# Performance work log

Hardware: AMD Instinct MI355X
Metric: run time of the kernel (lower is better)

The kernel has to match this reference:

```python
import jax, jax.numpy as jnp
import numpy as np

D = 512      # d_model
S = 8        # num_quantum_states
B, T = 16, 1024
LN_EPS = 1e-5


def setup_inputs() -> dict:
    key = jax.random.key(0)
    ks = jax.random.split(key, 10)
    sc = lambda fan_in: 1.0 / np.sqrt(fan_in)
    return {
        "x": jax.random.normal(ks[0], (B, T, D), dtype=jnp.float32),
        # entanglement gates: torch Linear weight [out=D, in=2D], bias [D], stacked over S
        "W_ent": jax.random.uniform(ks[1], (S, D, 2 * D), minval=-sc(2 * D), maxval=sc(2 * D)),
        "b_ent": jax.random.uniform(ks[2], (S, D), minval=-sc(2 * D), maxval=sc(2 * D)),
        # measurement MLP: Linear(D*S->D), LayerNorm(D), Tanh, Linear(D->1)
        "m1_w": jax.random.uniform(ks[3], (D, D * S), minval=-sc(D * S), maxval=sc(D * S)),
        "m1_b": jax.random.uniform(ks[4], (D,), minval=-sc(D * S), maxval=sc(D * S)),
        "ln_g": jnp.ones((D,), dtype=jnp.float32),
        "ln_b": jnp.zeros((D,), dtype=jnp.float32),
        "m2_w": jax.random.uniform(ks[5], (1, D), minval=-sc(D), maxval=sc(D)),
        "m2_b": jax.random.uniform(ks[6], (1,), minval=-sc(D), maxval=sc(D)),
    }


def _layernorm(h, g, b):
    mu = jnp.mean(h, axis=-1, keepdims=True)
    var = jnp.mean(jnp.square(h - mu), axis=-1, keepdims=True)
    return (h - mu) * jax.lax.rsqrt(var + LN_EPS) * g + b


def reference(x, W_ent, b_ent, m1_w, m1_b, ln_g, ln_b, m2_w, m2_b):
    b_, t_, d_ = x.shape
    s_ = W_ent.shape[0]
    # gate(cat[x_i, x_j]).mean(dim=2) == x_i @ W1^T + mean_j(x_j) @ W2^T + b  (exact algebra)
    W1 = W_ent[:, :, :d_]   # [S, D, D] acts on x_i
    W2 = W_ent[:, :, d_:]   # [S, D, D] acts on x_j (mean over j)
    xbar = jnp.mean(x, axis=1)                                   # [B, D]
    ent = (jnp.einsum('btd,sed->bste', x, W1)                    # [B, S, T, D]
           + jnp.einsum('bd,sed->bse', xbar, W2)[:, :, None, :]
           + b_ent[None, :, None, :])
    # permute(0,2,3,1).reshape(B,T,D*S): feature layout is (d, s) fastest on s
    qv = jnp.transpose(ent, (0, 2, 3, 1)).reshape(b_, t_, d_ * s_)
    h = jnp.tanh(_layernorm(qv @ m1_w.T + m1_b, ln_g, ln_b))     # [B, T, D]
    attn_logits = h @ m2_w.T + m2_b                              # [B, T, 1]
    attn_weights = jax.nn.softmax(attn_logits, axis=1)
    context = jnp.sum(attn_weights * x, axis=1)                  # [B, D]
    return context, attn_weights
```

## Files before the change

### kernel.cpp

```cpp
#include <hip/hip_runtime.h>
#include <hip/hip_bf16.h>

typedef __attribute__((ext_vector_type(8))) short bf16x8;
typedef __attribute__((ext_vector_type(4))) float f32x4;

__device__ __forceinline__ float bf2f(unsigned short u) {
    union { unsigned int i; float f; } c; c.i = ((unsigned int)u) << 16; return c.f;
}
__device__ __forceinline__ unsigned short f2bf(float f) {
    union { float f; unsigned int i; } c; c.f = f;
    unsigned int x = c.i;
    x += 0x7fffu + ((x >> 16) & 1u);
    return (unsigned short)(x >> 16);
}
__device__ __forceinline__ float tanh_fast(float v) {
    float a = fabsf(v);
    a = fminf(a, 15.0f);
    float e = __expf(2.0f * a);
    float t = 1.0f - 2.0f / (e + 1.0f);
    return copysignf(t, v);
}

#define GLOAD_LDS16(gp, lp) \
    __builtin_amdgcn_global_load_lds((const __attribute__((address_space(1))) void*)(gp), \
                                     (__attribute__((address_space(3))) void*)(lp), 16, 0, 0)

#define MFMA(a, b, c) __builtin_amdgcn_mfma_f32_16x16x32_bf16((a), (b), (c), 0, 0, 0)


__global__ void k_sumx(const float* __restrict__ x, float* __restrict__ sumx) {
    int b = blockIdx.x, tc = blockIdx.y;
    int tid = threadIdx.x;
    const float* xp = x + ((size_t)b * 1024 + tc * 64) * 512;
    float a0 = 0.f, a1 = 0.f;
    for (int t = 0; t < 64; ++t) {
        a0 += xp[(size_t)t * 512 + tid];
        a1 += xp[(size_t)t * 512 + tid + 256];
    }
    atomicAdd(&sumx[b * 512 + tid], a0);
    atomicAdd(&sumx[b * 512 + tid + 256], a1);
}

__global__ void k_prepA(const float* __restrict__ m1w, const float* __restrict__ bent,
                        unsigned short* __restrict__ Abf, float* __restrict__ bias2) {
    int i = blockIdx.x, tid = threadIdx.x;
    const float* row = m1w + (size_t)i * 4096;
    float acc = 0.f;
    #pragma unroll
    for (int q = 0; q < 4; ++q) {
        int col = q * 1024 + tid * 4;
        float4 v = *(const float4*)(row + col);
        ushort4 o;
        o.x = f2bf(v.x); o.y = f2bf(v.y); o.z = f2bf(v.z); o.w = f2bf(v.w);
        *(ushort4*)(Abf + (size_t)i * 4096 + col) = o;
        int e0 = col >> 3, s0 = col & 7;
        acc += v.x * bent[(s0    ) * 512 + e0];
        acc += v.y * bent[(s0 + 1) * 512 + e0];
        acc += v.z * bent[(s0 + 2) * 512 + e0];
        acc += v.w * bent[(s0 + 3) * 512 + e0];
    }
    #pragma unroll
    for (int off = 32; off; off >>= 1) acc += __shfl_xor(acc, off);
    __shared__ float r4[4];
    if ((tid & 63) == 0) r4[tid >> 6] = acc;
    __syncthreads();
    if (tid == 0) bias2[i] = r4[0] + r4[1] + r4[2] + r4[3];
}

__global__ void k_conv_W(const float* __restrict__ W, unsigned short* __restrict__ WT) {
    __shared__ float tile[128][33];
    int e0 = blockIdx.x * 16;
    int j0 = blockIdx.y * 32;
    int tid = threadIdx.x;
    int tx = tid & 31, ty = tid >> 5;
    #pragma unroll
    for (int q = 0; q < 16; ++q) {
        int lk = q * 8 + ty;
        int de = lk >> 3, s = lk & 7;
        int r = s * 512 + e0 + de;
        tile[lk][tx] = W[(size_t)r * 1024 + j0 + tx];
    }
    __syncthreads();
    int j = tid >> 3, ck = (tid & 7) * 16;
    unsigned short* dst = WT + (size_t)(j0 + j) * 4096 + e0 * 8 + ck;
    #pragma unroll
    for (int g = 0; g < 4; ++g) {
        ushort4 o;
        o.x = f2bf(tile[ck + g * 4 + 0][j]);
        o.y = f2bf(tile[ck + g * 4 + 1][j]);
        o.z = f2bf(tile[ck + g * 4 + 2][j]);
        o.w = f2bf(tile[ck + g * 4 + 3][j]);
        *(ushort4*)(dst + g * 4) = o;
    }
}

__launch_bounds__(512, 2)
__global__ void k_gemm1(const unsigned short* __restrict__ Abf,
                        const unsigned short* __restrict__ WT,
                        float* __restrict__ CpL, float* __restrict__ CpR) {
    __shared__ __align__(16) unsigned short sA[64 * 64];
    __shared__ __align__(16) unsigned short sB[256 * 64];
    int i0 = blockIdx.x * 64;
    int j0 = blockIdx.y * 256;
    int kbase = blockIdx.z * 512;
    int tid = threadIdx.x, lane = tid & 63, w = tid >> 6;
    int wm = w >> 2, wn = w & 3;
    int lr = lane >> 3, sl = lane & 7;
    int lo = lane & 15, hi = lane >> 4;
    int arow = w * 8 + lr;
    const unsigned short* gA = Abf + (size_t)(i0 + arow) * 4096 + kbase + ((sl ^ lr) << 3);
    unsigned short* dA = sA + w * 8 * 64;
    const unsigned short* gB[4]; unsigned short* dB[4];
    #pragma unroll
    for (int g = 0; g < 4; ++g) {
        int brow = w * 32 + g * 8 + lr;
        gB[g] = WT + (size_t)(j0 + brow) * 4096 + kbase + ((sl ^ lr) << 3);
        dB[g] = sB + (w * 32 + g * 8) * 64;
    }
    bool left = (blockIdx.y < 2);
    f32x4 acc[2][4] = {};
    for (int k0 = 0; k0 < 512; k0 += 64) {
        if (k0) __syncthreads();
        GLOAD_LDS16(gA + k0, dA);
        #pragma unroll
        for (int g = 0; g < 4; ++g) GLOAD_LDS16(gB[g] + k0, dB[g]);
        __syncthreads();
        #pragma unroll
        for (int kk = 0; kk < 2; ++kk) {
            int slotX = ((kk * 4 + hi) ^ (lo & 7)) << 3;
            bf16x8 a0 = *(const bf16x8*)(sA + (wm * 32 +      lo) * 64 + slotX);
            bf16x8 a1 = *(const bf16x8*)(sA + (wm * 32 + 16 + lo) * 64 + slotX);
            #pragma unroll
            for (int n = 0; n < 4; ++n) {
                bf16x8 bb = *(const bf16x8*)(sB + (wn * 64 + n * 16 + lo) * 64 + slotX);
                if (left) {
                    acc[0][n] = MFMA(a0, bb, acc[0][n]);
                    acc[1][n] = MFMA(a1, bb, acc[1][n]);
                } else {
                    acc[0][n] = MFMA(bb, a0, acc[0][n]);
                    acc[1][n] = MFMA(bb, a1, acc[1][n]);
                }
            }
        }
    }
    int ksoff = blockIdx.z * 262144;
    if (left) {
        #pragma unroll
        for (int m = 0; m < 2; ++m) {
            int ib = i0 + wm * 32 + m * 16 + hi * 4;
            #pragma unroll
            for (int n = 0; n < 4; ++n) {
                int j = j0 + wn * 64 + n * 16 + lo;
                #pragma unroll
                for (int r = 0; r < 4; ++r)
                    CpL[ksoff + (ib + r) * 512 + j] = acc[m][n][r];
            }
        }
    } else {
        #pragma unroll
        for (int m = 0; m < 2; ++m) {
            int ic = i0 + wm * 32 + m * 16 + lo;
            #pragma unroll
            for (int n = 0; n < 4; ++n) {
                int db = j0 - 512 + wn * 64 + n * 16 + hi * 4;
                #pragma unroll
                for (int r = 0; r < 4; ++r)
                    CpR[ksoff + (db + r) * 512 + ic] = acc[m][n][r];
            }
        }
    }
}

__global__ void k_reduce8(const float* __restrict__ Cp, unsigned short* __restrict__ outbf) {
    int gid = blockIdx.x * 256 + threadIdx.x;
    float4 s = ((const float4*)Cp)[gid];
    #pragma unroll
    for (int ks = 1; ks < 8; ++ks) {
        float4 t = ((const float4*)Cp)[ks * 65536 + gid];
        s.x += t.x; s.y += t.y; s.z += t.z; s.w += t.w;
    }
    ushort4 o;
    o.x = f2bf(s.x); o.y = f2bf(s.y); o.z = f2bf(s.z); o.w = f2bf(s.w);
    ((ushort4*)outbf)[gid] = o;
}

__global__ void k_cb(const float* __restrict__ sumx, const unsigned short* __restrict__ M2t,
                     const float* __restrict__ bias2, const float* __restrict__ m1b,
                     float* __restrict__ cbo) {
    int b = blockIdx.x, i0 = blockIdx.y * 64;
    int tid = threadIdx.x;
    int il = tid & 63, dq = tid >> 6;
    const float* sx = sumx + b * 512 + dq * 128;
    const unsigned short* mp = M2t + (size_t)dq * 128 * 512 + i0 + il;
    float acc = 0.f;
    #pragma unroll 4
    for (int dd = 0; dd < 128; ++dd)
        acc += sx[dd] * bf2f(mp[(size_t)dd * 512]);
    __shared__ float sPart[4][64];
    sPart[dq][il] = acc;
    __syncthreads();
    if (tid < 64) {
        float v = sPart[0][tid] + sPart[1][tid] + sPart[2][tid] + sPart[3][tid];
        cbo[b * 512 + i0 + tid] = v * (1.0f / 1024.0f) + bias2[i0 + tid] + m1b[i0 + tid];
    }
}

__launch_bounds__(512, 2)
__global__ void k_gemm2(const float* __restrict__ x,
                        const unsigned short* __restrict__ M1bf,
                        const float* __restrict__ cb,
                        const float* __restrict__ lng, const float* __restrict__ lnb,
                        const float* __restrict__ m2w, const float* __restrict__ m2b,
                        float* __restrict__ logits) {
    __shared__ __align__(16) unsigned short sA[64 * 64];
    __shared__ __align__(16) unsigned short sB[512 * 64];
    __shared__ float sRed[2][8][64];
    __shared__ float sMu[64], sRs[64];
    __shared__ float sLp[8][64];
    int bt0 = blockIdx.x * 64;
    int b = bt0 >> 10;
    int tid = threadIdx.x, lane = tid & 63, w = tid >> 6;
    int wm = w >> 2, wn = w & 3;
    int lo = lane & 15, hi = lane >> 4;
    int lr = lane >> 3, sl = lane & 7;
    int arow = tid >> 3, aslot = tid & 7;
    const float* gA = x + (size_t)(bt0 + arow) * 512 + aslot * 8;
    unsigned short* dAp = sA + arow * 64 + ((aslot ^ (arow & 7)) << 3);
    const unsigned short* gB[8]; unsigned short* dB[8];
    #pragma unroll
    for (int g = 0; g < 8; ++g) {
        int brow = w * 64 + g * 8 + lr;
        gB[g] = M1bf + (size_t)brow * 512 + ((sl ^ lr) << 3);
        dB[g] = sB + (w * 64 + g * 8) * 64;
    }
    f32x4 acc[2][8] = {};
    for (int k0 = 0; k0 < 512; k0 += 64) {
        if (k0) __syncthreads();
        #pragma unroll
        for (int g = 0; g < 8; ++g) GLOAD_LDS16(gB[g] + k0, dB[g]);
        float4 f0 = *(const float4*)(gA + k0);
        float4 f1 = *(const float4*)(gA + k0 + 4);
        bf16x8 pk;
        pk[0] = (short)f2bf(f0.x); pk[1] = (short)f2bf(f0.y);
        pk[2] = (short)f2bf(f0.z); pk[3] = (short)f2bf(f0.w);
        pk[4] = (short)f2bf(f1.x); pk[5] = (short)f2bf(f1.y);
        pk[6] = (short)f2bf(f1.z); pk[7] = (short)f2bf(f1.w);
        *(bf16x8*)dAp = pk;
        __syncthreads();
        #pragma unroll
        for (int kk = 0; kk < 2; ++kk) {
            int slotX = ((kk * 4 + hi) ^ (lo & 7)) << 3;
            bf16x8 a0 = *(const bf16x8*)(sA + (wm * 32 +      lo) * 64 + slotX);
            bf16x8 a1 = *(const bf16x8*)(sA + (wm * 32 + 16 + lo) * 64 + slotX);
            #pragma unroll
            for (int n = 0; n < 8; ++n) {
                bf16x8 bb = *(const bf16x8*)(sB + (wn * 128 + n * 16 + lo) * 64 + slotX);
                acc[0][n] = MFMA(a0, bb, acc[0][n]);
                acc[1][n] = MFMA(a1, bb, acc[1][n]);
            }
        }
    }
    #pragma unroll
    for (int n = 0; n < 8; ++n) {
        float cbv = cb[b * 512 + wn * 128 + n * 16 + lo];
        #pragma unroll
        for (int m = 0; m < 2; ++m)
            #pragma unroll
            for (int r = 0; r < 4; ++r)
                acc[m][n][r] += cbv;
    }
    #pragma unroll
    for (int m = 0; m < 2; ++m) {
        #pragma unroll
        for (int r = 0; r < 4; ++r) {
            float s1 = 0.f, s2 = 0.f;
            #pragma unroll
            for (int n = 0; n < 8; ++n) { float t = acc[m][n][r]; s1 += t; s2 += t * t; }
            #pragma unroll
            for (int msk = 1; msk < 16; msk <<= 1) {
                s1 += __shfl_xor(s1, msk);
                s2 += __shfl_xor(s2, msk);
            }
            if (lo == 0) {
                int row = wm * 32 + m * 16 + hi * 4 + r;
                sRed[0][w][row] = s1;
                sRed[1][w][row] = s2;
            }
        }
    }
    __syncthreads();
    if (tid < 64) {
        int wmr = tid >> 5;
        float s1 = 0.f, s2 = 0.f;
        #pragma unroll
        for (int q = 0; q < 4; ++q) { s1 += sRed[0][wmr * 4 + q][tid]; s2 += sRed[1][wmr * 4 + q][tid]; }
        float mu = s1 * (1.0f / 512.0f);
        float var = s2 * (1.0f / 512.0f) - mu * mu;
        sMu[tid] = mu;
        sRs[tid] = rsqrtf(var + 1e-5f);
    }
    __syncthreads();
    float gv[8], bv[8], wv[8];
    #pragma unroll
    for (int n = 0; n < 8; ++n) {
        int c = wn * 128 + n * 16 + lo;
        gv[n] = lng[c]; bv[n] = lnb[c]; wv[n] = m2w[c];
    }
    #pragma unroll
    for (int m = 0; m < 2; ++m) {
        #pragma unroll
        for (int r = 0; r < 4; ++r) {
            int row = wm * 32 + m * 16 + hi * 4 + r;
            float mu = sMu[row], rs = sRs[row];
            float lg = 0.f;
            #pragma unroll
            for (int n = 0; n < 8; ++n) {
                float h = tanh_fast((acc[m][n][r] - mu) * rs * gv[n] + bv[n]);
                lg += h * wv[n];
            }
            #pragma unroll
            for (int msk = 1; msk < 16; msk <<= 1) lg += __shfl_xor(lg, msk);
            if (lo == 0) sLp[w][row] = lg;
        }
    }
    __syncthreads();
    if (tid < 64) {
        int wmr = tid >> 5;
        float lg = 0.f;
        #pragma unroll
        for (int q = 0; q < 4; ++q) lg += sLp[wmr * 4 + q][tid];
        logits[bt0 + tid] = lg + m2b[0];
    }
}

__global__ void k_softmax(const float* __restrict__ logits, float* __restrict__ wout) {
    int b = blockIdx.x, tid = threadIdx.x;
    __shared__ float red[4];
    float4 v = ((const float4*)(logits + b * 1024))[tid];
    float mx = fmaxf(fmaxf(v.x, v.y), fmaxf(v.z, v.w));
    for (int off = 32; off; off >>= 1) mx = fmaxf(mx, __shfl_xor(mx, off));
    if ((tid & 63) == 0) red[tid >> 6] = mx;
    __syncthreads();
    mx = fmaxf(fmaxf(red[0], red[1]), fmaxf(red[2], red[3]));
    float e0 = expf(v.x - mx), e1 = expf(v.y - mx), e2 = expf(v.z - mx), e3 = expf(v.w - mx);
    float sm = e0 + e1 + e2 + e3;
    for (int off = 32; off; off >>= 1) sm += __shfl_xor(sm, off);
    __syncthreads();
    if ((tid & 63) == 0) red[tid >> 6] = sm;
    __syncthreads();
    float inv = 1.0f / (red[0] + red[1] + red[2] + red[3]);
    float4 o; o.x = e0 * inv; o.y = e1 * inv; o.z = e2 * inv; o.w = e3 * inv;
    ((float4*)(wout + b * 1024))[tid] = o;
}

__global__ void k_context(const float* __restrict__ x, const float* __restrict__ wts,
                          float* __restrict__ ctx) {
    int b = blockIdx.x, tc = blockIdx.y;
    int tid = threadIdx.x;
    const float* xp = x + ((size_t)b * 1024 + tc * 64) * 512;
    const float* wp = wts + b * 1024 + tc * 64;
    float a0 = 0.f, a1 = 0.f;
    for (int t = 0; t < 64; ++t) {
        float wv = wp[t];
        a0 += wv * xp[(size_t)t * 512 + tid];
        a1 += wv * xp[(size_t)t * 512 + tid + 256];
    }
    atomicAdd(&ctx[b * 512 + tid], a0);
    atomicAdd(&ctx[b * 512 + tid + 256], a1);
}

extern "C" void kernel_launch(void* const* d_in, const int* in_sizes, int n_in,
                              void* d_out, int out_size, void* d_ws, size_t ws_size,
                              hipStream_t stream) {
    (void)in_sizes; (void)n_in; (void)out_size; (void)ws_size;
    const float* x    = (const float*)d_in[0];
    const float* Went = (const float*)d_in[1];
    const float* bent = (const float*)d_in[2];
    const float* m1w  = (const float*)d_in[3];
    const float* m1b  = (const float*)d_in[4];
    const float* lng  = (const float*)d_in[5];
    const float* lnb  = (const float*)d_in[6];
    const float* m2w  = (const float*)d_in[7];
    const float* m2b  = (const float*)d_in[8];
    float* out = (float*)d_out;
    char* ws = (char*)d_ws;

    unsigned short* Abf   = (unsigned short*)(ws);
    unsigned short* WT    = (unsigned short*)(ws + 4194304);
    float* CpL            = (float*)(ws + 12582912);
    float* CpR            = (float*)(ws + 20971520);
    unsigned short* M1bf  = (unsigned short*)(ws + 29360128);
    unsigned short* M2t   = (unsigned short*)(ws + 29884416);
    float* sumx   = (float*)(ws + 30408704);
    float* bias2  = (float*)(ws + 30441472);
    float* cb     = (float*)(ws + 30443520);
    float* logits = (float*)(ws + 30476288);

    hipMemsetAsync(sumx, 0, 512 * 16 * sizeof(float), stream);
    hipMemsetAsync(out, 0, 8192 * sizeof(float), stream);

    k_sumx<<<dim3(16, 16), 256, 0, stream>>>(x, sumx);
    k_prepA<<<512, 256, 0, stream>>>(m1w, bent, Abf, bias2);
    k_conv_W<<<dim3(32, 32), 256, 0, stream>>>(Went, WT);
    k_gemm1<<<dim3(8, 4, 8), 512, 0, stream>>>(Abf, WT, CpL, CpR);
    k_reduce8<<<256, 256, 0, stream>>>(CpL, M1bf);
    k_reduce8<<<256, 256, 0, stream>>>(CpR, M2t);
    k_cb<<<dim3(16, 8), 256, 0, stream>>>(sumx, M2t, bias2, m1b, cb);
    k_gemm2<<<256, 512, 0, stream>>>(x, M1bf, cb, lng, lnb, m2w, m2b, logits);
    k_softmax<<<16, 256, 0, stream>>>(logits, out + 8192);
    k_context<<<dim3(16, 16), 256, 0, stream>>>(x, out + 8192, out);
}
```

Before: 93.73 us.

## Double-buffer LDS in both GEMMs and merge the two reduce launches

Both MFMA GEMM kernels now keep two LDS buffers and issue the global-to-LDS loads for the next k-tile before computing on the current one. Explicit vmcnt waits, raw barriers, sched barriers and setprio around the MFMA block control the ordering. The two split-K reduce launches are merged into one grid of 512 blocks. In exchange, gemm2 doubles its LDS use (about 72 KB per block), which may cut occupancy, and its launch bound drops the min-blocks hint. The hand-counted vmcnt values must stay in step with the number of loads issued.

New measurement: 90.34 us. -3.6%, faster.

```diff
diff --git a/kernel.cpp b/kernel.cpp
--- a/kernel.cpp
+++ b/kernel.cpp
@@ -26,6 +26,9 @@
                                      (__attribute__((address_space(3))) void*)(lp), 16, 0, 0)
 
 #define MFMA(a, b, c) __builtin_amdgcn_mfma_f32_16x16x32_bf16((a), (b), (c), 0, 0, 0)
+
+#define SBAR()  __builtin_amdgcn_s_barrier()
+#define SCHED0() __builtin_amdgcn_sched_barrier(0)
 
 
 __global__ void k_sumx(const float* __restrict__ x, float* __restrict__ sumx) {
@@ -98,8 +101,8 @@
 __global__ void k_gemm1(const unsigned short* __restrict__ Abf,
                         const unsigned short* __restrict__ WT,
                         float* __restrict__ CpL, float* __restrict__ CpR) {
-    __shared__ __align__(16) unsigned short sA[64 * 64];
-    __shared__ __align__(16) unsigned short sB[256 * 64];
+    __shared__ __align__(16) unsigned short sA[2][64 * 64];
+    __shared__ __align__(16) unsigned short sB[2][256 * 64];
     int i0 = blockIdx.x * 64;
     int j0 = blockIdx.y * 256;
     int kbase = blockIdx.z * 512;
@@ -109,30 +112,44 @@
     int lo = lane & 15, hi = lane >> 4;
     int arow = w * 8 + lr;
     const unsigned short* gA = Abf + (size_t)(i0 + arow) * 4096 + kbase + ((sl ^ lr) << 3);
-    unsigned short* dA = sA + w * 8 * 64;
-    const unsigned short* gB[4]; unsigned short* dB[4];
-    #pragma unroll
-    for (int g = 0; g < 4; ++g) {
-        int brow = w * 32 + g * 8 + lr;
-        gB[g] = WT + (size_t)(j0 + brow) * 4096 + kbase + ((sl ^ lr) << 3);
-        dB[g] = sB + (w * 32 + g * 8) * 64;
-    }
+    const unsigned short* gB0 = WT + (size_t)(j0 + w * 32 + 0 * 8 + lr) * 4096 + kbase + ((sl ^ lr) << 3);
+    const unsigned short* gB1 = WT + (size_t)(j0 + w * 32 + 1 * 8 + lr) * 4096 + kbase + ((sl ^ lr) << 3);
+    const unsigned short* gB2 = WT + (size_t)(j0 + w * 32 + 2 * 8 + lr) * 4096 + kbase + ((sl ^ lr) << 3);
+    const unsigned short* gB3 = WT + (size_t)(j0 + w * 32 + 3 * 8 + lr) * 4096 + kbase + ((sl ^ lr) << 3);
     bool left = (blockIdx.y < 2);
     f32x4 acc[2][4] = {};
-    for (int k0 = 0; k0 < 512; k0 += 64) {
-        if (k0) __syncthreads();
-        GLOAD_LDS16(gA + k0, dA);
-        #pragma unroll
-        for (int g = 0; g < 4; ++g) GLOAD_LDS16(gB[g] + k0, dB[g]);
-        __syncthreads();
+
+#define G1_STAGE(tt, bufn)                                                    \
+    do {                                                                      \
+        int koff = (tt) * 64;                                                 \
+        GLOAD_LDS16(gA + koff, &sA[bufn][w * 8 * 64]);                        \
+        GLOAD_LDS16(gB0 + koff, &sB[bufn][(w * 32 + 0) * 64]);                \
+        GLOAD_LDS16(gB1 + koff, &sB[bufn][(w * 32 + 8) * 64]);                \
+        GLOAD_LDS16(gB2 + koff, &sB[bufn][(w * 32 + 16) * 64]);               \
+        GLOAD_LDS16(gB3 + koff, &sB[bufn][(w * 32 + 24) * 64]);               \
+        SCHED0();                                                             \
+    } while (0)
+
+    G1_STAGE(0, 0);
+    #pragma unroll
+    for (int t = 0; t < 8; ++t) {
+        int buf = t & 1;
+        if (t < 7) {
+            G1_STAGE(t + 1, buf ^ 1);
+            asm volatile("s_waitcnt vmcnt(5)" ::: "memory");
+        } else {
+            asm volatile("s_waitcnt vmcnt(0)" ::: "memory");
+        }
+        SCHED0(); SBAR(); SCHED0();
+        __builtin_amdgcn_s_setprio(1);
         #pragma unroll
         for (int kk = 0; kk < 2; ++kk) {
             int slotX = ((kk * 4 + hi) ^ (lo & 7)) << 3;
-            bf16x8 a0 = *(const bf16x8*)(sA + (wm * 32 +      lo) * 64 + slotX);
-            bf16x8 a1 = *(const bf16x8*)(sA + (wm * 32 + 16 + lo) * 64 + slotX);
+            bf16x8 a0 = *(const bf16x8*)(&sA[buf][(wm * 32 +      lo) * 64 + slotX]);
+            bf16x8 a1 = *(const bf16x8*)(&sA[buf][(wm * 32 + 16 + lo) * 64 + slotX]);
             #pragma unroll
             for (int n = 0; n < 4; ++n) {
-                bf16x8 bb = *(const bf16x8*)(sB + (wn * 64 + n * 16 + lo) * 64 + slotX);
+                bf16x8 bb = *(const bf16x8*)(&sB[buf][(wn * 64 + n * 16 + lo) * 64 + slotX]);
                 if (left) {
                     acc[0][n] = MFMA(a0, bb, acc[0][n]);
                     acc[1][n] = MFMA(a1, bb, acc[1][n]);
@@ -142,7 +159,11 @@
                 }
             }
         }
-    }
+        __builtin_amdgcn_s_setprio(0);
+        if (t < 7) { SCHED0(); SBAR(); SCHED0(); }
+    }
+#undef G1_STAGE
+
     int ksoff = blockIdx.z * 262144;
     if (left) {
         #pragma unroll
@@ -171,8 +192,12 @@
     }
 }
 
-__global__ void k_reduce8(const float* __restrict__ Cp, unsigned short* __restrict__ outbf) {
-    int gid = blockIdx.x * 256 + threadIdx.x;
+__global__ void k_reduce(const float* __restrict__ CpL, const float* __restrict__ CpR,
+                         unsigned short* __restrict__ M1bf, unsigned short* __restrict__ M2t) {
+    int bx = blockIdx.x;
+    const float* Cp = (bx < 256) ? CpL : CpR;
+    unsigned short* ob = (bx < 256) ? M1bf : M2t;
+    int gid = (bx & 255) * 256 + threadIdx.x;
     float4 s = ((const float4*)Cp)[gid];
     #pragma unroll
     for (int ks = 1; ks < 8; ++ks) {
@@ -181,7 +206,7 @@
     }
     ushort4 o;
     o.x = f2bf(s.x); o.y = f2bf(s.y); o.z = f2bf(s.z); o.w = f2bf(s.w);
-    ((ushort4*)outbf)[gid] = o;
+    ((ushort4*)ob)[gid] = o;
 }
 
 __global__ void k_cb(const float* __restrict__ sumx, const unsigned short* __restrict__ M2t,
@@ -205,15 +230,15 @@
     }
 }
 
-__launch_bounds__(512, 2)
+__launch_bounds__(512)
 __global__ void k_gemm2(const float* __restrict__ x,
                         const unsigned short* __restrict__ M1bf,
                         const float* __restrict__ cb,
                         const float* __restrict__ lng, const float* __restrict__ lnb,
                         const float* __restrict__ m2w, const float* __restrict__ m2b,
                         float* __restrict__ logits) {
-    __shared__ __align__(16) unsigned short sA[64 * 64];
-    __shared__ __align__(16) unsigned short sB[512 * 64];
+    __shared__ __align__(16) unsigned short sA[2][64 * 64];
+    __shared__ __align__(16) unsigned short sB[2][512 * 64];
     __shared__ float sRed[2][8][64];
     __shared__ float sMu[64], sRs[64];
     __shared__ float sLp[8][64];
@@ -225,41 +250,77 @@
     int lr = lane >> 3, sl = lane & 7;
     int arow = tid >> 3, aslot = tid & 7;
     const float* gA = x + (size_t)(bt0 + arow) * 512 + aslot * 8;
-    unsigned short* dAp = sA + arow * 64 + ((aslot ^ (arow & 7)) << 3);
-    const unsigned short* gB[8]; unsigned short* dB[8];
-    #pragma unroll
-    for (int g = 0; g < 8; ++g) {
-        int brow = w * 64 + g * 8 + lr;
-        gB[g] = M1bf + (size_t)brow * 512 + ((sl ^ lr) << 3);
-        dB[g] = sB + (w * 64 + g * 8) * 64;
-    }
+    int aoff = arow * 64 + ((aslot ^ (arow & 7)) << 3);
+    const unsigned short* gB[8];
+    #pragma unroll
+    for (int g = 0; g < 8; ++g)
+        gB[g] = M1bf + (size_t)(w * 64 + g * 8 + lr) * 512 + ((sl ^ lr) << 3);
+    float4 pf0, pf1;
     f32x4 acc[2][8] = {};
-    for (int k0 = 0; k0 < 512; k0 += 64) {
-        if (k0) __syncthreads();
-        #pragma unroll
-        for (int g = 0; g < 8; ++g) GLOAD_LDS16(gB[g] + k0, dB[g]);
-        float4 f0 = *(const float4*)(gA + k0);
-        float4 f1 = *(const float4*)(gA + k0 + 4);
-        bf16x8 pk;
-        pk[0] = (short)f2bf(f0.x); pk[1] = (short)f2bf(f0.y);
-        pk[2] = (short)f2bf(f0.z); pk[3] = (short)f2bf(f0.w);
-        pk[4] = (short)f2bf(f1.x); pk[5] = (short)f2bf(f1.y);
-        pk[6] = (short)f2bf(f1.z); pk[7] = (short)f2bf(f1.w);
-        *(bf16x8*)dAp = pk;
-        __syncthreads();
+
+#define G2_ISSUE(tt, bufn)                                                    \
+    do {                                                                      \
+        pf0 = *(const float4*)(gA + (tt) * 64);                               \
+        pf1 = *(const float4*)(gA + (tt) * 64 + 4);                           \
+        SCHED0();                                                             \
+        _Pragma("unroll")                                                     \
+        for (int g = 0; g < 8; ++g)                                           \
+            GLOAD_LDS16(gB[g] + (tt) * 64, &sB[bufn][(w * 64 + g * 8) * 64]); \
+        SCHED0();                                                             \
+    } while (0)
+
+#define G2_AWRITE(bufn)                                                      \
+    do {                                                                     \
+        bf16x8 pk;                                                           \
+        pk[0] = (short)f2bf(pf0.x); pk[1] = (short)f2bf(pf0.y);              \
+        pk[2] = (short)f2bf(pf0.z); pk[3] = (short)f2bf(pf0.w);              \
+        pk[4] = (short)f2bf(pf1.x); pk[5] = (short)f2bf(pf1.y);              \
+        pk[6] = (short)f2bf(pf1.z); pk[7] = (short)f2bf(pf1.w);              \
+        *(bf16x8*)(&sA[bufn][aoff]) = pk;                                    \
+    } while (0)
+
+    G2_ISSUE(0, 0);
+    asm volatile("s_waitcnt vmcnt(8)" ::: "memory");
+    SCHED0();
+    G2_AWRITE(0);
+    asm volatile("s_waitcnt lgkmcnt(0)" ::: "memory");
+    SCHED0();
+
+    #pragma unroll
+    for (int t = 0; t < 8; ++t) {
+        int buf = t & 1;
+        if (t < 7) {
+            G2_ISSUE(t + 1, buf ^ 1);
+            asm volatile("s_waitcnt vmcnt(10)" ::: "memory");
+        } else {
+            asm volatile("s_waitcnt vmcnt(0)" ::: "memory");
+        }
+        SCHED0(); SBAR(); SCHED0();
+        __builtin_amdgcn_s_setprio(1);
         #pragma unroll
         for (int kk = 0; kk < 2; ++kk) {
             int slotX = ((kk * 4 + hi) ^ (lo & 7)) << 3;
-            bf16x8 a0 = *(const bf16x8*)(sA + (wm * 32 +      lo) * 64 + slotX);
-            bf16x8 a1 = *(const bf16x8*)(sA + (wm * 32 + 16 + lo) * 64 + slotX);
+            bf16x8 a0 = *(const bf16x8*)(&sA[buf][(wm * 32 +      lo) * 64 + slotX]);
+            bf16x8 a1 = *(const bf16x8*)(&sA[buf][(wm * 32 + 16 + lo) * 64 + slotX]);
             #pragma unroll
             for (int n = 0; n < 8; ++n) {
-                bf16x8 bb = *(const bf16x8*)(sB + (wn * 128 + n * 16 + lo) * 64 + slotX);
+                bf16x8 bb = *(const bf16x8*)(&sB[buf][(wn * 128 + n * 16 + lo) * 64 + slotX]);
                 acc[0][n] = MFMA(a0, bb, acc[0][n]);
                 acc[1][n] = MFMA(a1, bb, acc[1][n]);
             }
         }
-    }
+        __builtin_amdgcn_s_setprio(0);
+        if (t < 7) {
+            asm volatile("s_waitcnt vmcnt(8)" ::: "memory");
+            SCHED0();
+            G2_AWRITE(buf ^ 1);
+            asm volatile("s_waitcnt lgkmcnt(0)" ::: "memory");
+            SCHED0(); SBAR(); SCHED0();
+        }
+    }
+#undef G2_ISSUE
+#undef G2_AWRITE
+
     #pragma unroll
     for (int n = 0; n < 8; ++n) {
         float cbv = cb[b * 512 + wn * 128 + n * 16 + lo];
@@ -403,8 +464,7 @@
     k_prepA<<<512, 256, 0, stream>>>(m1w, bent, Abf, bias2);
     k_conv_W<<<dim3(32, 32), 256, 0, stream>>>(Went, WT);
     k_gemm1<<<dim3(8, 4, 8), 512, 0, stream>>>(Abf, WT, CpL, CpR);
-    k_reduce8<<<256, 256, 0, stream>>>(CpL, M1bf);
-    k_reduce8<<<256, 256, 0, stream>>>(CpR, M2t);
+    k_reduce<<<512, 256, 0, stream>>>(CpL, CpR, M1bf, M2t);
     k_cb<<<dim3(16, 8), 256, 0, stream>>>(sumx, M2t, bias2, m1b, cb);
     k_gemm2<<<256, 512, 0, stream>>>(x, M1bf, cb, lng, lnb, m2w, m2b, logits);
     k_softmax<<<16, 256, 0, stream>>>(logits, out + 8192);
```
